# Performance work log

Measured on AMD Instinct MI355X. Metric: run time of the kernel, lower is better.

## Reference

```python
import jax, jax.numpy as jnp
import numpy as np

N_NODES = 50000
N_EDGES = 200000
NODE_F = 64
EDGE_F = 16
HID = 32
LAT = 16


def _glorot(key, shape):
    fan_in, fan_out = shape[0], shape[1]
    lim = np.sqrt(6.0 / (fan_in + fan_out))
    return jax.random.uniform(key, shape, jnp.float32, -lim, lim)


def setup_inputs() -> dict:
    key = jax.random.key(0)
    ks = jax.random.split(key, 24)
    inp = {
        "x": jax.random.normal(ks[0], (N_NODES, NODE_F), jnp.float32),
        "edge_index": jax.random.randint(ks[1], (2, N_EDGES), 0, N_NODES, jnp.int64),
        "edge_attr": jax.random.normal(ks[2], (N_EDGES, EDGE_F), jnp.float32),
        # encoder input projection
        "lin_in_w": _glorot(ks[3], (NODE_F, HID)),
        "lin_in_b": jnp.zeros((HID,), jnp.float32),
        # 3 edge MLPs (stacked over layer axis)
        "edge_w1": jnp.stack([_glorot(ks[4 + i], (EDGE_F, HID)) for i in range(3)]),
        "edge_b1": jnp.zeros((3, HID), jnp.float32),
        "edge_w2": jnp.stack([_glorot(ks[7 + i], (HID, HID * HID)) * 0.1 for i in range(3)]),
        "edge_b2": jnp.zeros((3, HID * HID), jnp.float32),
        # 3 NNConv root weights + biases
        "root_w": jnp.stack([_glorot(ks[10 + i], (HID, HID)) for i in range(3)]),
        "root_b": jnp.zeros((3, HID), jnp.float32),
        # encoder output projection
        "lin_out_w": _glorot(ks[13], (HID, LAT)),
        "lin_out_b": jnp.zeros((LAT,), jnp.float32),
        # node decoder MLP
        "dec_w1": _glorot(ks[14], (LAT, HID)),
        "dec_b1": jnp.zeros((HID,), jnp.float32),
        "dec_w2": _glorot(ks[15], (HID, NODE_F)),
        "dec_b2": jnp.zeros((NODE_F,), jnp.float32),
    }
    return inp


def _nnconv(x, src, dst, edge_attr, w1, b1, w2, b2, root_w, root_b):
    # per-edge weight matrix from edge MLP: [E, H, H]
    h = jax.nn.relu(edge_attr @ w1 + b1)
    w_e = (h @ w2 + b2).reshape(-1, HID, HID)
    # gather source features, per-edge matmul: [E, H]
    msg = jnp.einsum("eh,eho->eo", x[src], w_e)
    # scatter-mean to destinations
    agg = jax.ops.segment_sum(msg, dst, num_segments=N_NODES)
    cnt = jax.ops.segment_sum(jnp.ones((msg.shape[0], 1), x.dtype), dst, num_segments=N_NODES)
    agg = agg / jnp.maximum(cnt, 1.0)
    # root weight + bias
    return agg + x @ root_w + root_b


def reference(x, edge_index, edge_attr, lin_in_w, lin_in_b, edge_w1, edge_b1,
              edge_w2, edge_b2, root_w, root_b, lin_out_w, lin_out_b,
              dec_w1, dec_b1, dec_w2, dec_b2):
    src, dst = edge_index[0], edge_index[1]
    h = jax.nn.relu(x @ lin_in_w + lin_in_b)
    for i in range(3):  # fixed number of conv layers (dropout is identity in eval)
        h = _nnconv(h, src, dst, edge_attr, edge_w1[i], edge_b1[i],
                    edge_w2[i], edge_b2[i], root_w[i], root_b[i])
        h = jax.nn.relu(h)
    z = h @ lin_out_w + lin_out_b
    # node decoder
    d = jax.nn.relu(z @ dec_w1 + dec_b1)
    return d @ dec_w2 + dec_b2
```

## Files before the change

kernel.cpp:

```cpp
#include <hip/hip_runtime.h>
#include <hip/hip_bf16.h>
#include <stdint.h>

#define N_NODES 50000
#define N_EDGES 200000
#define NODE_F 64
#define EDGE_F 16
#define HID 32
#define LAT 16
#define W2A_L 33792
#define SCAN_BLOCKS 196

typedef __attribute__((ext_vector_type(8))) short short8;
typedef __attribute__((ext_vector_type(4))) float f32x4;
typedef __attribute__((ext_vector_type(2))) float f32x2;

static __device__ __forceinline__ unsigned short bfbits(float f) {
  union { __hip_bfloat16 h; unsigned short s; } c; c.h = __float2bfloat16(f); return c.s;
}
static __device__ __forceinline__ unsigned pkt(f32x2 v) {
  return __builtin_amdgcn_perm(__float_as_uint(v.y), __float_as_uint(v.x), 0x07060302u);
}
union AFrag { short8 v; unsigned u[4]; };

__global__ void k_prep(const float* __restrict__ ew2, const float* __restrict__ eb2,
                       const float* __restrict__ ew1,
                       unsigned short* __restrict__ w2a,
                       unsigned short* __restrict__ w1p,
                       int* __restrict__ deg,
                       float* __restrict__ agg) {
  int g = blockIdx.x*256 + threadIdx.x;
  int l = g / W2A_L;
  int r = g % W2A_L;
  int k = r >> 10;
  int r2 = r & 1023;
  int mt = r2 >> 9;
  int ln = (r2 >> 3) & 63;
  int j  = r2 & 7;
  int h  = (ln >> 4)*8 + j;
  int m  = mt*16 + (ln & 15);
  float v = (k < 32) ? ew2[(size_t)l*32768 + k*1024 + h*32 + m]
                     : eb2[(size_t)l*1024 + h*32 + m];
  w2a[g] = bfbits(v);
  if (g < N_NODES) deg[g] = 0;
  {
    float4 z4 = make_float4(0.f,0.f,0.f,0.f);
    float4* a4 = (float4*)agg;
    for (int i = g; i < N_NODES*HID/4; i += 101376) a4[i] = z4;
  }
  if (g < 3*2*64*8) {
    int l2 = g >> 10;
    int r3 = g & 1023;
    int nt = r3 >> 9;
    int ln2 = (r3 >> 3) & 63;
    int j2  = r3 & 7;
    int kgr = ln2 >> 4;
    float w = (kgr < 2) ? ew1[(size_t)l2*512 + (kgr*8 + j2)*32 + nt*16 + (ln2 & 15)] : 0.f;
    w1p[g] = bfbits(w);
  }
}

__global__ void k_hist(const int* __restrict__ ei, int* __restrict__ deg) {
  int t = blockIdx.x*256 + threadIdx.x;
  if (t >= N_EDGES) return;
  int d = ei[N_EDGES + t];
  d = min(max(d, 0), N_NODES-1);
  atomicAdd(&deg[d], 1);
}

__global__ __launch_bounds__(256) void k_scan1(const int* __restrict__ deg,
                                               int* __restrict__ off,
                                               int* __restrict__ bsum) {
  __shared__ int s[256];
  const int tid = threadIdx.x;
  const int t = blockIdx.x*256 + tid;
  int d = (t < N_NODES) ? deg[t] : 0;
  s[tid] = d; __syncthreads();
  int v = d;
  #pragma unroll
  for (int ofs = 1; ofs < 256; ofs <<= 1) {
    int w = (tid >= ofs) ? s[tid-ofs] : 0;
    __syncthreads();
    v += w; s[tid] = v;
    __syncthreads();
  }
  if (t < N_NODES) off[t] = v - d;
  if (tid == 255) bsum[blockIdx.x] = v;
}

__global__ __launch_bounds__(256) void k_scan23(int* __restrict__ off,
                                                const int* __restrict__ bsum,
                                                int* __restrict__ cursor) {
  __shared__ int sPref;
  const int tid = threadIdx.x;
  const int b = blockIdx.x;
  if (tid < 64) {
    int acc = 0;
    for (int i = tid; i < b; i += 64) acc += bsum[i];
    #pragma unroll
    for (int o = 32; o; o >>= 1) acc += __shfl_down(acc, o);
    if (tid == 0) sPref = acc;
  }
  __syncthreads();
  int pref = sPref;
  int t = b*256 + tid;
  if (t < N_NODES) {
    off[t] += pref;
    cursor[t] = 0;
  }
  if (t == 0) off[N_NODES] = N_EDGES;
}

__global__ void k_scatter(const int* __restrict__ ei, const int* __restrict__ off,
                          int* __restrict__ cursor,
                          int* __restrict__ csr_src, int* __restrict__ csr_eid,
                          int* __restrict__ csr_dst) {
  int t = blockIdx.x*256 + threadIdx.x;
  if (t >= N_EDGES) return;
  int d = ei[N_EDGES + t];
  d = min(max(d, 0), N_NODES-1);
  int s = ei[t];
  s = min(max(s, 0), N_NODES-1);
  int pos = off[d] + atomicAdd(&cursor[d], 1);
  csr_src[pos] = s;
  csr_eid[pos] = t;
  csr_dst[pos] = d;
}

__global__ void k_lin_in(const float* __restrict__ x,
                         const float* __restrict__ W,
                         const float* __restrict__ b,
                         float* __restrict__ h) {
  __shared__ float Ws[NODE_F*HID];
  __shared__ float bs[HID];
  for (int i = threadIdx.x; i < NODE_F*HID; i += 256) Ws[i] = W[i];
  if (threadIdx.x < HID) bs[threadIdx.x] = b[threadIdx.x];
  __syncthreads();
  int t = blockIdx.x*256 + threadIdx.x;
  if (t >= N_NODES*HID) return;
  int n = t >> 5, o = t & 31;
  const float4* xp = (const float4*)(x + (size_t)n*NODE_F);
  float acc = bs[o];
  #pragma unroll
  for (int j = 0; j < NODE_F/4; j++) {
    float4 v = xp[j];
    acc = fmaf(v.x, Ws[(4*j+0)*HID+o], acc);
    acc = fmaf(v.y, Ws[(4*j+1)*HID+o], acc);
    acc = fmaf(v.z, Ws[(4*j+2)*HID+o], acc);
    acc = fmaf(v.w, Ws[(4*j+3)*HID+o], acc);
  }
  h[t] = fmaxf(acc, 0.f);
}

__global__ __launch_bounds__(256) void k_msgagg(const float* __restrict__ hin,
                                                const float* __restrict__ ea,
                                                const unsigned short* __restrict__ w1pl,
                                                const float* __restrict__ b1,
                                                const unsigned short* __restrict__ w2al,
                                                const int* __restrict__ csr_src,
                                                const int* __restrict__ csr_eid,
                                                const int* __restrict__ csr_dst,
                                                const int* __restrict__ off,
                                                float* __restrict__ agg) {
  __shared__ float sHE[256*33];
  __shared__ int   sSRC[256];
  __shared__ int   sEID[256];
  const int tid = threadIdx.x;
  const int be  = blockIdx.x*256;
  const int wv   = tid >> 6;
  const int lane = tid & 63;
  const int nn   = lane & 15;
  const int quad = lane >> 4;
  const int wbase = wv*64;

  {
    int el = wbase + lane;
    int pos = min(be + el, N_EDGES-1);
    sSRC[el] = csr_src[pos];
    sEID[el] = csr_eid[pos];
    sHE[el*33 + 32] = 1.0f;
  }

  {
    short8 wb0 = *(const short8*)(w1pl + lane*8);
    short8 wb1 = *(const short8*)(w1pl + 512 + lane*8);
    f32x4 z = {0.f,0.f,0.f,0.f};
    float bv0 = b1[nn], bv1 = b1[nn + 16];
    #pragma unroll
    for (int t = 0; t < 4; t++) {
      AFrag a;
      if (quad < 2) {
        int e = sEID[wbase + t*16 + nn];
        const float4* p = (const float4*)(ea + (size_t)e*EDGE_F + quad*8);
        float4 u = p[0], v = p[1];
        a.u[0] = pkt(f32x2{u.x,u.y}); a.u[1] = pkt(f32x2{u.z,u.w});
        a.u[2] = pkt(f32x2{v.x,v.y}); a.u[3] = pkt(f32x2{v.z,v.w});
      } else {
        #pragma unroll
        for (int i = 0; i < 4; i++) a.u[i] = 0u;
      }
      f32x4 h0 = __builtin_amdgcn_mfma_f32_16x16x32_bf16(a.v, wb0, z, 0, 0, 0);
      f32x4 h1 = __builtin_amdgcn_mfma_f32_16x16x32_bf16(a.v, wb1, z, 0, 0, 0);
      #pragma unroll
      for (int r = 0; r < 4; r++) {
        int ro = (wbase + t*16 + quad*4 + r)*33;
        sHE[ro + nn]      = fmaxf(h0[r] + bv0, 0.f);
        sHE[ro + 16 + nn] = fmaxf(h1[r] + bv1, 0.f);
      }
    }
  }

  short8 bx[4];
  #pragma unroll
  for (int t = 0; t < 4; t++) {
    int si = sSRC[wbase + t*16 + nn];
    const float4* p = (const float4*)(hin + (size_t)si*HID + quad*8);
    float4 a = p[0], b = p[1];
    AFrag f;
    f.u[0] = pkt(f32x2{a.x,a.y}); f.u[1] = pkt(f32x2{a.z,a.w});
    f.u[2] = pkt(f32x2{b.x,b.y}); f.u[3] = pkt(f32x2{b.z,b.w});
    bx[t] = f.v;
  }

  f32x4 c0[4], c1[4];
  #pragma unroll
  for (int t = 0; t < 4; t++) { c0[t] = f32x4{0.f,0.f,0.f,0.f}; c1[t] = c0[t]; }
  const f32x4 zz = {0.f,0.f,0.f,0.f};

  const unsigned short* ap = w2al + (unsigned)lane*8;
  const float* heR[4];
  #pragma unroll
  for (int t = 0; t < 4; t++) heR[t] = sHE + (wbase + t*16 + nn)*33;

  short8 sa0[3], sa1[3];
  float  sh[3][4];
  #pragma unroll
  for (int j = 0; j < 3; j++) {
    sa0[j] = *(const short8*)(ap + j*1024);
    sa1[j] = *(const short8*)(ap + j*1024 + 512);
    #pragma unroll
    for (int t = 0; t < 4; t++) sh[j][t] = heR[t][j];
  }

  #pragma unroll 1
  for (int base = 0; base < 30; base += 3) {
    #pragma unroll
    for (int j = 0; j < 3; j++) {
      const int kk = base + j;
      short8 a0 = sa0[j], a1 = sa1[j];
      #pragma unroll
      for (int t = 0; t < 4; t++) {
        f32x4 u0 = __builtin_amdgcn_mfma_f32_16x16x32_bf16(a0, bx[t], zz, 0, 0, 0);
        f32x4 u1 = __builtin_amdgcn_mfma_f32_16x16x32_bf16(a1, bx[t], zz, 0, 0, 0);
        float hk = sh[j][t];
        #pragma unroll
        for (int r = 0; r < 4; r++) {
          c0[t][r] = fmaf(hk, u0[r], c0[t][r]);
          c1[t][r] = fmaf(hk, u1[r], c1[t][r]);
        }
      }
      sa0[j] = *(const short8*)(ap + (kk+3)*1024);
      sa1[j] = *(const short8*)(ap + (kk+3)*1024 + 512);
      #pragma unroll
      for (int t = 0; t < 4; t++) sh[j][t] = heR[t][kk+3];
    }
  }
  #pragma unroll
  for (int j = 0; j < 3; j++) {
    short8 a0 = sa0[j], a1 = sa1[j];
    #pragma unroll
    for (int t = 0; t < 4; t++) {
      f32x4 u0 = __builtin_amdgcn_mfma_f32_16x16x32_bf16(a0, bx[t], zz, 0, 0, 0);
      f32x4 u1 = __builtin_amdgcn_mfma_f32_16x16x32_bf16(a1, bx[t], zz, 0, 0, 0);
      float hk = sh[j][t];
      #pragma unroll
      for (int r = 0; r < 4; r++) {
        c0[t][r] = fmaf(hk, u0[r], c0[t][r]);
        c1[t][r] = fmaf(hk, u1[r], c1[t][r]);
      }
    }
  }

  #pragma unroll
  for (int t = 0; t < 4; t++) {
    int ro = (wbase + t*16 + nn)*33 + quad*4;
    sHE[ro + 0]  = c0[t][0]; sHE[ro + 1]  = c0[t][1];
    sHE[ro + 2]  = c0[t][2]; sHE[ro + 3]  = c0[t][3];
    sHE[ro + 16] = c1[t][0]; sHE[ro + 17] = c1[t][1];
    sHE[ro + 18] = c1[t][2]; sHE[ro + 19] = c1[t][3];
  }
  __syncthreads();

  const int s    = be;
  const int wend = s + 256;
  const int nF = csr_dst[min(s,       N_EDGES-1)];
  const int nL = csr_dst[min(s + 255, N_EDGES-1)];
  for (int basei = 0; basei <= nL - nF; basei += 32) {
    int idx = basei + (tid >> 3);
    int n = nF + idx;
    if (n <= nL) {
      int oc = tid & 7;
      int s0 = off[n], s1 = off[n+1];
      int lo = max(s0, s) - s;
      int hi = min(s1, wend) - s;
      float a0 = 0.f, a1 = 0.f, a2 = 0.f, a3 = 0.f;
      for (int j = lo; j < hi; j++) {
        const float* row = sHE + j*33 + oc*4;
        a0 += row[0]; a1 += row[1]; a2 += row[2]; a3 += row[3];
      }
      float* dst = agg + (size_t)n*HID + oc*4;
      if (s0 >= s && s1 <= wend) {
        *(float4*)dst = make_float4(a0, a1, a2, a3);
      } else {
        atomicAdd(dst + 0, a0); atomicAdd(dst + 1, a1);
        atomicAdd(dst + 2, a2); atomicAdd(dst + 3, a3);
      }
    }
  }
}

__global__ void k_root(float* __restrict__ agg,
                       const int* __restrict__ off,
                       const float* __restrict__ hin,
                       const float* __restrict__ rw,
                       const float* __restrict__ rb,
                       float* __restrict__ hout) {
  __shared__ float rws[HID*HID];
  __shared__ float rbs[HID];
  for (int i = threadIdx.x; i < HID*HID; i += 256) rws[i] = rw[i];
  if (threadIdx.x < HID) rbs[threadIdx.x] = rb[threadIdx.x];
  __syncthreads();
  int t = blockIdx.x*256 + threadIdx.x;
  if (t >= N_NODES*8) return;
  int n = t >> 3, oc = t & 7;
  float4* ap = (float4*)(agg + (size_t)n*HID);
  float4 av = ap[oc];
  float inv = 1.f / fmaxf((float)(off[n+1] - off[n]), 1.f);
  float a0 = fmaf(av.x, inv, rbs[oc*4+0]);
  float a1 = fmaf(av.y, inv, rbs[oc*4+1]);
  float a2 = fmaf(av.z, inv, rbs[oc*4+2]);
  float a3 = fmaf(av.w, inv, rbs[oc*4+3]);
  const float4* hp = (const float4*)(hin + (size_t)n*HID);
  #pragma unroll
  for (int jq = 0; jq < 8; jq++) {
    float4 hv = hp[jq];
    #pragma unroll
    for (int c = 0; c < 4; c++) {
      int j = jq*4 + c;
      float h = (c==0)?hv.x:(c==1)?hv.y:(c==2)?hv.z:hv.w;
      const float4* rp = (const float4*)(rws + j*HID + oc*4);
      float4 r = rp[0];
      a0 = fmaf(h, r.x, a0);
      a1 = fmaf(h, r.y, a1);
      a2 = fmaf(h, r.z, a2);
      a3 = fmaf(h, r.w, a3);
    }
  }
  ((float4*)(hout + (size_t)n*HID))[oc] =
      make_float4(fmaxf(a0,0.f), fmaxf(a1,0.f), fmaxf(a2,0.f), fmaxf(a3,0.f));
  ap[oc] = make_float4(0.f, 0.f, 0.f, 0.f);
}

__global__ void k_decoder(const float* __restrict__ agg,
                          const int* __restrict__ off,
                          const float* __restrict__ h,
                          const float* __restrict__ rw, const float* __restrict__ rb,
                          const float* __restrict__ lo_w, const float* __restrict__ lo_b,
                          const float* __restrict__ d1_w, const float* __restrict__ d1_b,
                          const float* __restrict__ d2_w, const float* __restrict__ d2_b,
                          float* __restrict__ out) {
  __shared__ float rws[HID*HID], rbs[HID];
  __shared__ float lows[HID*LAT], lobs[LAT], d1s[LAT*HID], d1bs[HID], d2s[HID*NODE_F], d2bs[NODE_F];
  for (int i = threadIdx.x; i < HID*HID; i += 256) rws[i] = rw[i];
  for (int i = threadIdx.x; i < HID; i += 256) rbs[i] = rb[i];
  for (int i = threadIdx.x; i < HID*LAT; i += 256) lows[i] = lo_w[i];
  for (int i = threadIdx.x; i < LAT; i += 256) lobs[i] = lo_b[i];
  for (int i = threadIdx.x; i < LAT*HID; i += 256) d1s[i] = d1_w[i];
  for (int i = threadIdx.x; i < HID; i += 256) d1bs[i] = d1_b[i];
  for (int i = threadIdx.x; i < HID*NODE_F; i += 256) d2s[i] = d2_w[i];
  for (int i = threadIdx.x; i < NODE_F; i += 256) d2bs[i] = d2_b[i];
  __syncthreads();
  int n = blockIdx.x*256 + threadIdx.x;
  if (n >= N_NODES) return;
  float hv[HID], av[HID];
  const float4* hp = (const float4*)(h + (size_t)n*HID);
  const float4* ap = (const float4*)(agg + (size_t)n*HID);
  #pragma unroll
  for (int i = 0; i < HID/4; i++) {
    float4 v = hp[i]; hv[4*i]=v.x; hv[4*i+1]=v.y; hv[4*i+2]=v.z; hv[4*i+3]=v.w;
    float4 a = ap[i]; av[4*i]=a.x; av[4*i+1]=a.y; av[4*i+2]=a.z; av[4*i+3]=a.w;
  }
  float inv = 1.f / fmaxf((float)(off[n+1] - off[n]), 1.f);
  float hr[HID];
  #pragma unroll 4
  for (int o = 0; o < HID; o++) {
    float a = fmaf(av[o], inv, rbs[o]);
    #pragma unroll
    for (int j = 0; j < HID; j++) a = fmaf(hv[j], rws[j*HID+o], a);
    hr[o] = fmaxf(a, 0.f);
  }
  float z[LAT];
  #pragma unroll
  for (int o = 0; o < LAT; o++) {
    float a = lobs[o];
    #pragma unroll
    for (int j = 0; j < HID; j++) a = fmaf(hr[j], lows[j*LAT+o], a);
    z[o] = a;
  }
  float d[HID];
  #pragma unroll
  for (int o = 0; o < HID; o++) {
    float a = d1bs[o];
    #pragma unroll
    for (int j = 0; j < LAT; j++) a = fmaf(z[j], d1s[j*HID+o], a);
    d[o] = fmaxf(a, 0.f);
  }
  float* op = out + (size_t)n*NODE_F;
  #pragma unroll 8
  for (int o = 0; o < NODE_F; o++) {
    float a = d2bs[o];
    #pragma unroll
    for (int j = 0; j < HID; j++) a = fmaf(d[j], d2s[j*NODE_F+o], a);
    op[o] = a;
  }
}

extern "C" void kernel_launch(void* const* d_in, const int* in_sizes, int n_in,
                              void* d_out, int out_size, void* d_ws, size_t ws_size,
                              hipStream_t stream) {
  const float* x   = (const float*)d_in[0];
  const int*   ei  = (const int*)d_in[1];
  const float* ea  = (const float*)d_in[2];
  const float* liw = (const float*)d_in[3];
  const float* lib = (const float*)d_in[4];
  const float* ew1 = (const float*)d_in[5];
  const float* eb1 = (const float*)d_in[6];
  const float* ew2 = (const float*)d_in[7];
  const float* eb2 = (const float*)d_in[8];
  const float* rw  = (const float*)d_in[9];
  const float* rb  = (const float*)d_in[10];
  const float* low = (const float*)d_in[11];
  const float* lob = (const float*)d_in[12];
  const float* d1w = (const float*)d_in[13];
  const float* d1b = (const float*)d_in[14];
  const float* d2w = (const float*)d_in[15];
  const float* d2b = (const float*)d_in[16];
  float* out = (float*)d_out;

  float* h0   = (float*)d_ws;
  float* h1   = h0  + (size_t)N_NODES*HID;
  float* agg  = h1  + (size_t)N_NODES*HID;
  int*  deg   = (int*)(agg + (size_t)N_NODES*HID);
  int*  off   = deg + N_NODES;
  int*  cursor= off + N_NODES + 16;
  int*  csrs  = cursor + N_NODES;
  int*  csre  = csrs + N_EDGES;
  int*  csrd  = csre + N_EDGES;
  int*  bsum  = csrd + N_EDGES;
  unsigned short* w2a = (unsigned short*)(bsum + 256);
  unsigned short* w1p = w2a + 3*W2A_L;

  k_prep<<<(3*W2A_L)/256, 256, 0, stream>>>(ew2, eb2, ew1, w2a, w1p, deg, agg);
  k_hist<<<(N_EDGES + 255)/256, 256, 0, stream>>>(ei, deg);
  k_scan1<<<SCAN_BLOCKS, 256, 0, stream>>>(deg, off, bsum);
  k_scan23<<<SCAN_BLOCKS, 256, 0, stream>>>(off, bsum, cursor);
  k_scatter<<<(N_EDGES + 255)/256, 256, 0, stream>>>(ei, off, cursor, csrs, csre, csrd);

  k_lin_in<<<(N_NODES*HID + 255)/256, 256, 0, stream>>>(x, liw, lib, h0);

  k_msgagg<<<(N_EDGES + 255)/256, 256, 0, stream>>>(h0, ea, w1p, eb1,
      w2a, csrs, csre, csrd, off, agg);
  k_root<<<(N_NODES*8 + 255)/256, 256, 0, stream>>>(agg, off, h0, rw, rb, h1);
  k_msgagg<<<(N_EDGES + 255)/256, 256, 0, stream>>>(h1, ea, w1p + 1024, eb1 + HID,
      w2a + (size_t)W2A_L, csrs, csre, csrd, off, agg);
  k_root<<<(N_NODES*8 + 255)/256, 256, 0, stream>>>(agg, off, h1, rw + HID*HID, rb + HID, h0);
  k_msgagg<<<(N_EDGES + 255)/256, 256, 0, stream>>>(h0, ea, w1p + 2048, eb1 + 2*HID,
      w2a + (size_t)2*W2A_L, csrs, csre, csrd, off, agg);
  k_decoder<<<(N_NODES + 255)/256, 256, 0, stream>>>(agg, off, h0,
      rw + 2*HID*HID, rb + 2*HID, low, lob, d1w, d1b, d2w, d2b, out);
}
```

Baseline: 284.7 us.

## Fuse whole GNN pipeline into one persistent cooperative kernel with grid syncs

Replaces the chain of separate launches (prep, histogram, scan, scatter, input projection, three message/aggregate layers, root updates and decoder) with one cooperative kernel of 512 blocks. Stages are separated by grid-wide barriers, and the work loops are grid-strided. The goal is to remove per-launch overhead and the idle gaps between small kernels. The trade-off is the cost of about ten grid barriers, a fixed grid that processes the 782 message tiles in uneven rounds, and occupancy limited by the launch bound. The old multi-kernel path stays as a fallback if the cooperative launch fails.

```diff
diff --git a/kernel.cpp b/kernel.cpp
--- a/kernel.cpp
+++ b/kernel.cpp
@@ -1,4 +1,5 @@
 #include <hip/hip_runtime.h>
+#include <hip/hip_cooperative_groups.h>
 #include <hip/hip_bf16.h>
 #include <stdint.h>
 
@@ -10,6 +11,11 @@
 #define LAT 16
 #define W2A_L 33792
 #define SCAN_BLOCKS 196
+#define NTILES 782
+#define FUSED_BLOCKS 512
+#define FUSED_THREADS (FUSED_BLOCKS*256)
+
+namespace cg = cooperative_groups;
 
 typedef __attribute__((ext_vector_type(8))) short short8;
 typedef __attribute__((ext_vector_type(4))) float f32x4;
@@ -23,31 +29,25 @@
 }
 union AFrag { short8 v; unsigned u[4]; };
 
-__global__ void k_prep(const float* __restrict__ ew2, const float* __restrict__ eb2,
-                       const float* __restrict__ ew1,
-                       unsigned short* __restrict__ w2a,
-                       unsigned short* __restrict__ w1p,
-                       int* __restrict__ deg,
-                       float* __restrict__ agg) {
-  int g = blockIdx.x*256 + threadIdx.x;
-  int l = g / W2A_L;
-  int r = g % W2A_L;
-  int k = r >> 10;
-  int r2 = r & 1023;
-  int mt = r2 >> 9;
-  int ln = (r2 >> 3) & 63;
-  int j  = r2 & 7;
-  int h  = (ln >> 4)*8 + j;
-  int m  = mt*16 + (ln & 15);
-  float v = (k < 32) ? ew2[(size_t)l*32768 + k*1024 + h*32 + m]
-                     : eb2[(size_t)l*1024 + h*32 + m];
-  w2a[g] = bfbits(v);
+
+__device__ __forceinline__ void dev_prep_item(int g,
+    const float* ew2, const float* eb2, const float* ew1,
+    unsigned short* w2a, unsigned short* w1p, int* deg) {
+  if (g < 3*W2A_L) {
+    int l = g / W2A_L;
+    int r = g % W2A_L;
+    int k = r >> 10;
+    int r2 = r & 1023;
+    int mt = r2 >> 9;
+    int ln = (r2 >> 3) & 63;
+    int j  = r2 & 7;
+    int h  = (ln >> 4)*8 + j;
+    int m  = mt*16 + (ln & 15);
+    float v = (k < 32) ? ew2[(size_t)l*32768 + k*1024 + h*32 + m]
+                       : eb2[(size_t)l*1024 + h*32 + m];
+    w2a[g] = bfbits(v);
+  }
   if (g < N_NODES) deg[g] = 0;
-  {
-    float4 z4 = make_float4(0.f,0.f,0.f,0.f);
-    float4* a4 = (float4*)agg;
-    for (int i = g; i < N_NODES*HID/4; i += 101376) a4[i] = z4;
-  }
   if (g < 3*2*64*8) {
     int l2 = g >> 10;
     int r3 = g & 1023;
@@ -60,84 +60,8 @@
   }
 }
 
-__global__ void k_hist(const int* __restrict__ ei, int* __restrict__ deg) {
-  int t = blockIdx.x*256 + threadIdx.x;
-  if (t >= N_EDGES) return;
-  int d = ei[N_EDGES + t];
-  d = min(max(d, 0), N_NODES-1);
-  atomicAdd(&deg[d], 1);
-}
-
-__global__ __launch_bounds__(256) void k_scan1(const int* __restrict__ deg,
-                                               int* __restrict__ off,
-                                               int* __restrict__ bsum) {
-  __shared__ int s[256];
-  const int tid = threadIdx.x;
-  const int t = blockIdx.x*256 + tid;
-  int d = (t < N_NODES) ? deg[t] : 0;
-  s[tid] = d; __syncthreads();
-  int v = d;
-  #pragma unroll
-  for (int ofs = 1; ofs < 256; ofs <<= 1) {
-    int w = (tid >= ofs) ? s[tid-ofs] : 0;
-    __syncthreads();
-    v += w; s[tid] = v;
-    __syncthreads();
-  }
-  if (t < N_NODES) off[t] = v - d;
-  if (tid == 255) bsum[blockIdx.x] = v;
-}
-
-__global__ __launch_bounds__(256) void k_scan23(int* __restrict__ off,
-                                                const int* __restrict__ bsum,
-                                                int* __restrict__ cursor) {
-  __shared__ int sPref;
-  const int tid = threadIdx.x;
-  const int b = blockIdx.x;
-  if (tid < 64) {
-    int acc = 0;
-    for (int i = tid; i < b; i += 64) acc += bsum[i];
-    #pragma unroll
-    for (int o = 32; o; o >>= 1) acc += __shfl_down(acc, o);
-    if (tid == 0) sPref = acc;
-  }
-  __syncthreads();
-  int pref = sPref;
-  int t = b*256 + tid;
-  if (t < N_NODES) {
-    off[t] += pref;
-    cursor[t] = 0;
-  }
-  if (t == 0) off[N_NODES] = N_EDGES;
-}
-
-__global__ void k_scatter(const int* __restrict__ ei, const int* __restrict__ off,
-                          int* __restrict__ cursor,
-                          int* __restrict__ csr_src, int* __restrict__ csr_eid,
-                          int* __restrict__ csr_dst) {
-  int t = blockIdx.x*256 + threadIdx.x;
-  if (t >= N_EDGES) return;
-  int d = ei[N_EDGES + t];
-  d = min(max(d, 0), N_NODES-1);
-  int s = ei[t];
-  s = min(max(s, 0), N_NODES-1);
-  int pos = off[d] + atomicAdd(&cursor[d], 1);
-  csr_src[pos] = s;
-  csr_eid[pos] = t;
-  csr_dst[pos] = d;
-}
-
-__global__ void k_lin_in(const float* __restrict__ x,
-                         const float* __restrict__ W,
-                         const float* __restrict__ b,
-                         float* __restrict__ h) {
-  __shared__ float Ws[NODE_F*HID];
-  __shared__ float bs[HID];
-  for (int i = threadIdx.x; i < NODE_F*HID; i += 256) Ws[i] = W[i];
-  if (threadIdx.x < HID) bs[threadIdx.x] = b[threadIdx.x];
-  __syncthreads();
-  int t = blockIdx.x*256 + threadIdx.x;
-  if (t >= N_NODES*HID) return;
+__device__ __forceinline__ void dev_lin_item(int t, const float* x,
+    const float* Ws, const float* bs, float* h) {
   int n = t >> 5, o = t & 31;
   const float4* xp = (const float4*)(x + (size_t)n*NODE_F);
   float acc = bs[o];
@@ -152,21 +76,68 @@
   h[t] = fmaxf(acc, 0.f);
 }
 
-__global__ __launch_bounds__(256) void k_msgagg(const float* __restrict__ hin,
-                                                const float* __restrict__ ea,
-                                                const unsigned short* __restrict__ w1pl,
-                                                const float* __restrict__ b1,
-                                                const unsigned short* __restrict__ w2al,
-                                                const int* __restrict__ csr_src,
-                                                const int* __restrict__ csr_eid,
-                                                const int* __restrict__ csr_dst,
-                                                const int* __restrict__ off,
-                                                float* __restrict__ agg) {
-  __shared__ float sHE[256*33];
-  __shared__ int   sSRC[256];
-  __shared__ int   sEID[256];
-  const int tid = threadIdx.x;
-  const int be  = blockIdx.x*256;
+__device__ __forceinline__ void dev_hist_item(int t, const int* ei, int* deg) {
+  int d = ei[N_EDGES + t];
+  d = min(max(d, 0), N_NODES-1);
+  atomicAdd(&deg[d], 1);
+}
+
+__device__ __forceinline__ void dev_scan1(int b, int tid, int* s,
+    const int* deg, int* off, int* bsum) {
+  int t = b*256 + tid;
+  int d = (t < N_NODES) ? deg[t] : 0;
+  s[tid] = d; __syncthreads();
+  int v = d;
+  #pragma unroll
+  for (int ofs = 1; ofs < 256; ofs <<= 1) {
+    int w = (tid >= ofs) ? s[tid-ofs] : 0;
+    __syncthreads();
+    v += w; s[tid] = v;
+    __syncthreads();
+  }
+  if (t < N_NODES) off[t] = v - d;
+  if (tid == 255) bsum[b] = v;
+}
+
+__device__ __forceinline__ void dev_scan23(int b, int tid, int* sPref,
+    int* off, const int* bsum, int* cursor) {
+  if (tid < 64) {
+    int acc = 0;
+    for (int i = tid; i < b; i += 64) acc += bsum[i];
+    #pragma unroll
+    for (int o = 32; o; o >>= 1) acc += __shfl_down(acc, o);
+    if (tid == 0) sPref[0] = acc;
+  }
+  __syncthreads();
+  int pref = sPref[0];
+  int t = b*256 + tid;
+  if (t < N_NODES) {
+    off[t] += pref;
+    cursor[t] = 0;
+  }
+  if (t == 0) off[N_NODES] = N_EDGES;
+}
+
+__device__ __forceinline__ void dev_scatter_item(int t, const int* ei,
+    const int* off, int* cursor, int* csrs, int* csre, int* csrd) {
+  int d = ei[N_EDGES + t];
+  d = min(max(d, 0), N_NODES-1);
+  int s = ei[t];
+  s = min(max(s, 0), N_NODES-1);
+  int pos = off[d] + atomicAdd(&cursor[d], 1);
+  csrs[pos] = s;
+  csre[pos] = t;
+  csrd[pos] = d;
+}
+
+__device__ __forceinline__ void dev_msgagg_tile(
+    float* sHE, int* sSRC, int* sEID, int tile, int tid,
+    const float* hin, const float* ea,
+    const unsigned short* w1pl, const float* b1,
+    const unsigned short* w2al,
+    const int* csr_src, const int* csr_eid, const int* csr_dst,
+    const int* off, float* agg) {
+  const int be  = tile*256;
   const int wv   = tid >> 6;
   const int lane = tid & 63;
   const int nn   = lane & 15;
@@ -319,6 +290,261 @@
   }
 }
 
+__device__ __forceinline__ void dev_root_item(int t, float* agg, const int* off,
+    const float* hin, const float* rws, const float* rbs, float* hout) {
+  int n = t >> 3, oc = t & 7;
+  float4* ap = (float4*)(agg + (size_t)n*HID);
+  float4 av = ap[oc];
+  float inv = 1.f / fmaxf((float)(off[n+1] - off[n]), 1.f);
+  float a0 = fmaf(av.x, inv, rbs[oc*4+0]);
+  float a1 = fmaf(av.y, inv, rbs[oc*4+1]);
+  float a2 = fmaf(av.z, inv, rbs[oc*4+2]);
+  float a3 = fmaf(av.w, inv, rbs[oc*4+3]);
+  const float4* hp = (const float4*)(hin + (size_t)n*HID);
+  #pragma unroll
+  for (int jq = 0; jq < 8; jq++) {
+    float4 hv = hp[jq];
+    #pragma unroll
+    for (int c = 0; c < 4; c++) {
+      int j = jq*4 + c;
+      float h = (c==0)?hv.x:(c==1)?hv.y:(c==2)?hv.z:hv.w;
+      const float4* rp = (const float4*)(rws + j*HID + oc*4);
+      float4 r = rp[0];
+      a0 = fmaf(h, r.x, a0);
+      a1 = fmaf(h, r.y, a1);
+      a2 = fmaf(h, r.z, a2);
+      a3 = fmaf(h, r.w, a3);
+    }
+  }
+  ((float4*)(hout + (size_t)n*HID))[oc] =
+      make_float4(fmaxf(a0,0.f), fmaxf(a1,0.f), fmaxf(a2,0.f), fmaxf(a3,0.f));
+  ap[oc] = make_float4(0.f, 0.f, 0.f, 0.f);
+}
+
+__device__ __forceinline__ void dev_decoder_node(int n,
+    const float* agg, const int* off, const float* h,
+    const float* rws, const float* rbs,
+    const float* lows, const float* lobs,
+    const float* d1s, const float* d1bs,
+    const float* d2s, const float* d2bs,
+    float* out) {
+  float hv[HID], av[HID];
+  const float4* hp = (const float4*)(h + (size_t)n*HID);
+  const float4* ap = (const float4*)(agg + (size_t)n*HID);
+  #pragma unroll
+  for (int i = 0; i < HID/4; i++) {
+    float4 v = hp[i]; hv[4*i]=v.x; hv[4*i+1]=v.y; hv[4*i+2]=v.z; hv[4*i+3]=v.w;
+    float4 a = ap[i]; av[4*i]=a.x; av[4*i+1]=a.y; av[4*i+2]=a.z; av[4*i+3]=a.w;
+  }
+  float inv = 1.f / fmaxf((float)(off[n+1] - off[n]), 1.f);
+  float hr[HID];
+  #pragma unroll 4
+  for (int o = 0; o < HID; o++) {
+    float a = fmaf(av[o], inv, rbs[o]);
+    #pragma unroll
+    for (int j = 0; j < HID; j++) a = fmaf(hv[j], rws[j*HID+o], a);
+    hr[o] = fmaxf(a, 0.f);
+  }
+  float z[LAT];
+  #pragma unroll
+  for (int o = 0; o < LAT; o++) {
+    float a = lobs[o];
+    #pragma unroll
+    for (int j = 0; j < HID; j++) a = fmaf(hr[j], lows[j*LAT+o], a);
+    z[o] = a;
+  }
+  float d[HID];
+  #pragma unroll
+  for (int o = 0; o < HID; o++) {
+    float a = d1bs[o];
+    #pragma unroll
+    for (int j = 0; j < LAT; j++) a = fmaf(z[j], d1s[j*HID+o], a);
+    d[o] = fmaxf(a, 0.f);
+  }
+  float* op = out + (size_t)n*NODE_F;
+  #pragma unroll 8
+  for (int o = 0; o < NODE_F; o++) {
+    float a = d2bs[o];
+    #pragma unroll
+    for (int j = 0; j < HID; j++) a = fmaf(d[j], d2s[j*NODE_F+o], a);
+    op[o] = a;
+  }
+}
+
+
+struct FusedArgs {
+  const float *x, *ea;
+  const int *ei;
+  const float *liw, *lib, *eb1, *rw, *rb, *low, *lob, *d1w, *d1b, *d2w, *d2b;
+  const float *ew1, *ew2, *eb2;
+  float *out, *h0, *h1, *agg;
+  int *deg, *off, *cursor, *csrs, *csre, *csrd, *bsum;
+  unsigned short *w2a, *w1p;
+};
+
+__global__ __launch_bounds__(256, 2) void k_fused(FusedArgs a) {
+  __shared__ float smem[256*33 + 512];
+  cg::grid_group grid = cg::this_grid();
+  const int tid = threadIdx.x;
+  const int bid = blockIdx.x;
+  const int gidx = bid*256 + tid;
+
+  {
+    float* Ws = smem;
+    float* bs = smem + NODE_F*HID;
+    for (int i = tid; i < NODE_F*HID; i += 256) Ws[i] = a.liw[i];
+    if (tid < HID) bs[tid] = a.lib[tid];
+    __syncthreads();
+    dev_prep_item(gidx, a.ew2, a.eb2, a.ew1, a.w2a, a.w1p, a.deg);
+    float4 z4 = make_float4(0.f,0.f,0.f,0.f);
+    float4* a4 = (float4*)a.agg;
+    for (int i = gidx; i < N_NODES*HID/4; i += FUSED_THREADS) a4[i] = z4;
+    for (int t = gidx; t < N_NODES*HID; t += FUSED_THREADS)
+      dev_lin_item(t, a.x, Ws, bs, a.h0);
+  }
+  grid.sync();
+
+  for (int t = gidx; t < N_EDGES; t += FUSED_THREADS) dev_hist_item(t, a.ei, a.deg);
+  grid.sync();
+
+  if (bid < SCAN_BLOCKS) dev_scan1(bid, tid, (int*)smem, a.deg, a.off, a.bsum);
+  grid.sync();
+
+  if (bid < SCAN_BLOCKS) dev_scan23(bid, tid, (int*)smem, a.off, a.bsum, a.cursor);
+  grid.sync();
+
+  for (int t = gidx; t < N_EDGES; t += FUSED_THREADS)
+    dev_scatter_item(t, a.ei, a.off, a.cursor, a.csrs, a.csre, a.csrd);
+  grid.sync();
+
+  float* sHE = smem;
+  int* sSRC = (int*)(smem + 256*33);
+  int* sEID = sSRC + 256;
+  const float* hin = a.h0;
+  float* hout = a.h1;
+  #pragma unroll 1
+  for (int l = 0; l < 3; l++) {
+    const unsigned short* w1pl = a.w1p + (size_t)l*1024;
+    const float* b1 = a.eb1 + l*HID;
+    const unsigned short* w2al = a.w2a + (size_t)l*W2A_L;
+    #pragma unroll 1
+    for (int t5 = bid; t5 < NTILES; t5 += gridDim.x) {
+      __syncthreads();
+      dev_msgagg_tile(sHE, sSRC, sEID, t5, tid, hin, a.ea, w1pl, b1, w2al,
+                      a.csrs, a.csre, a.csrd, a.off, a.agg);
+    }
+    grid.sync();
+    if (l < 2) {
+      float* rws = smem;
+      float* rbs = smem + HID*HID;
+      for (int i = tid; i < HID*HID; i += 256) rws[i] = a.rw[(size_t)l*HID*HID + i];
+      if (tid < HID) rbs[tid] = a.rb[l*HID + tid];
+      __syncthreads();
+      for (int t = gidx; t < N_NODES*8; t += FUSED_THREADS)
+        dev_root_item(t, a.agg, a.off, hin, rws, rbs, hout);
+      grid.sync();
+      const float* tmp = hin; hin = hout; hout = (float*)tmp;
+    }
+  }
+
+  {
+    float* rws  = smem;
+    float* rbs  = smem + 1024;
+    float* lows = smem + 1056;
+    float* lobs = smem + 1568;
+    float* d1s  = smem + 1584;
+    float* d1bs = smem + 2096;
+    float* d2s  = smem + 2128;
+    float* d2bs = smem + 4176;
+    for (int i = tid; i < HID*HID; i += 256) rws[i] = a.rw[(size_t)2*HID*HID + i];
+    for (int i = tid; i < HID; i += 256) rbs[i] = a.rb[2*HID + i];
+    for (int i = tid; i < HID*LAT; i += 256) lows[i] = a.low[i];
+    for (int i = tid; i < LAT; i += 256) lobs[i] = a.lob[i];
+    for (int i = tid; i < LAT*HID; i += 256) d1s[i] = a.d1w[i];
+    for (int i = tid; i < HID; i += 256) d1bs[i] = a.d1b[i];
+    for (int i = tid; i < HID*NODE_F; i += 256) d2s[i] = a.d2w[i];
+    for (int i = tid; i < NODE_F; i += 256) d2bs[i] = a.d2b[i];
+    __syncthreads();
+    if (gidx < N_NODES)
+      dev_decoder_node(gidx, a.agg, a.off, hin, rws, rbs, lows, lobs,
+                       d1s, d1bs, d2s, d2bs, a.out);
+  }
+}
+
+
+__global__ void k_prep(const float* __restrict__ ew2, const float* __restrict__ eb2,
+                       const float* __restrict__ ew1,
+                       unsigned short* __restrict__ w2a,
+                       unsigned short* __restrict__ w1p,
+                       int* __restrict__ deg,
+                       float* __restrict__ agg) {
+  int g = blockIdx.x*256 + threadIdx.x;
+  dev_prep_item(g, ew2, eb2, ew1, w2a, w1p, deg);
+  float4 z4 = make_float4(0.f,0.f,0.f,0.f);
+  float4* a4 = (float4*)agg;
+  for (int i = g; i < N_NODES*HID/4; i += 101376) a4[i] = z4;
+}
+
+__global__ void k_hist(const int* __restrict__ ei, int* __restrict__ deg) {
+  int t = blockIdx.x*256 + threadIdx.x;
+  if (t >= N_EDGES) return;
+  dev_hist_item(t, ei, deg);
+}
+
+__global__ __launch_bounds__(256) void k_scan1(const int* __restrict__ deg,
+                                               int* __restrict__ off,
+                                               int* __restrict__ bsum) {
+  __shared__ int s[256];
+  dev_scan1(blockIdx.x, threadIdx.x, s, deg, off, bsum);
+}
+
+__global__ __launch_bounds__(256) void k_scan23(int* __restrict__ off,
+                                                const int* __restrict__ bsum,
+                                                int* __restrict__ cursor) {
+  __shared__ int sPref[1];
+  dev_scan23(blockIdx.x, threadIdx.x, sPref, off, bsum, cursor);
+}
+
+__global__ void k_scatter(const int* __restrict__ ei, const int* __restrict__ off,
+                          int* __restrict__ cursor,
+                          int* __restrict__ csr_src, int* __restrict__ csr_eid,
+                          int* __restrict__ csr_dst) {
+  int t = blockIdx.x*256 + threadIdx.x;
+  if (t >= N_EDGES) return;
+  dev_scatter_item(t, ei, off, cursor, csr_src, csr_eid, csr_dst);
+}
+
+__global__ void k_lin_in(const float* __restrict__ x,
+                         const float* __restrict__ W,
+                         const float* __restrict__ b,
+                         float* __restrict__ h) {
+  __shared__ float Ws[NODE_F*HID];
+  __shared__ float bs[HID];
+  for (int i = threadIdx.x; i < NODE_F*HID; i += 256) Ws[i] = W[i];
+  if (threadIdx.x < HID) bs[threadIdx.x] = b[threadIdx.x];
+  __syncthreads();
+  int t = blockIdx.x*256 + threadIdx.x;
+  if (t >= N_NODES*HID) return;
+  dev_lin_item(t, x, Ws, bs, h);
+}
+
+__global__ __launch_bounds__(256) void k_msgagg(const float* __restrict__ hin,
+                                                const float* __restrict__ ea,
+                                                const unsigned short* __restrict__ w1pl,
+                                                const float* __restrict__ b1,
+                                                const unsigned short* __restrict__ w2al,
+                                                const int* __restrict__ csr_src,
+                                                const int* __restrict__ csr_eid,
+                                                const int* __restrict__ csr_dst,
+                                                const int* __restrict__ off,
+                                                float* __restrict__ agg) {
+  __shared__ float sHE[256*33];
+  __shared__ int   sSRC[256];
+  __shared__ int   sEID[256];
+  dev_msgagg_tile(sHE, sSRC, sEID, blockIdx.x, threadIdx.x, hin, ea, w1pl, b1,
+                  w2al, csr_src, csr_eid, csr_dst, off, agg);
+}
+
 __global__ void k_root(float* __restrict__ agg,
                        const int* __restrict__ off,
                        const float* __restrict__ hin,
@@ -332,33 +558,7 @@
   __syncthreads();
   int t = blockIdx.x*256 + threadIdx.x;
   if (t >= N_NODES*8) return;
-  int n = t >> 3, oc = t & 7;
-  float4* ap = (float4*)(agg + (size_t)n*HID);
-  float4 av = ap[oc];
-  float inv = 1.f / fmaxf((float)(off[n+1] - off[n]), 1.f);
-  float a0 = fmaf(av.x, inv, rbs[oc*4+0]);
-  float a1 = fmaf(av.y, inv, rbs[oc*4+1]);
-  float a2 = fmaf(av.z, inv, rbs[oc*4+2]);
-  float a3 = fmaf(av.w, inv, rbs[oc*4+3]);
-  const float4* hp = (const float4*)(hin + (size_t)n*HID);
-  #pragma unroll
-  for (int jq = 0; jq < 8; jq++) {
-    float4 hv = hp[jq];
-    #pragma unroll
-    for (int c = 0; c < 4; c++) {
-      int j = jq*4 + c;
-      float h = (c==0)?hv.x:(c==1)?hv.y:(c==2)?hv.z:hv.w;
-      const float4* rp = (const float4*)(rws + j*HID + oc*4);
-      float4 r = rp[0];
-      a0 = fmaf(h, r.x, a0);
-      a1 = fmaf(h, r.y, a1);
-      a2 = fmaf(h, r.z, a2);
-      a3 = fmaf(h, r.w, a3);
-    }
-  }
-  ((float4*)(hout + (size_t)n*HID))[oc] =
-      make_float4(fmaxf(a0,0.f), fmaxf(a1,0.f), fmaxf(a2,0.f), fmaxf(a3,0.f));
-  ap[oc] = make_float4(0.f, 0.f, 0.f, 0.f);
+  dev_root_item(t, agg, off, hin, rws, rbs, hout);
 }
 
 __global__ void k_decoder(const float* __restrict__ agg,
@@ -382,47 +582,7 @@
   __syncthreads();
   int n = blockIdx.x*256 + threadIdx.x;
   if (n >= N_NODES) return;
-  float hv[HID], av[HID];
-  const float4* hp = (const float4*)(h + (size_t)n*HID);
-  const float4* ap = (const float4*)(agg + (size_t)n*HID);
-  #pragma unroll
-  for (int i = 0; i < HID/4; i++) {
-    float4 v = hp[i]; hv[4*i]=v.x; hv[4*i+1]=v.y; hv[4*i+2]=v.z; hv[4*i+3]=v.w;
-    float4 a = ap[i]; av[4*i]=a.x; av[4*i+1]=a.y; av[4*i+2]=a.z; av[4*i+3]=a.w;
-  }
-  float inv = 1.f / fmaxf((float)(off[n+1] - off[n]), 1.f);
-  float hr[HID];
-  #pragma unroll 4
-  for (int o = 0; o < HID; o++) {
-    float a = fmaf(av[o], inv, rbs[o]);
-    #pragma unroll
-    for (int j = 0; j < HID; j++) a = fmaf(hv[j], rws[j*HID+o], a);
-    hr[o] = fmaxf(a, 0.f);
-  }
-  float z[LAT];
-  #pragma unroll
-  for (int o = 0; o < LAT; o++) {
-    float a = lobs[o];
-    #pragma unroll
-    for (int j = 0; j < HID; j++) a = fmaf(hr[j], lows[j*LAT+o], a);
-    z[o] = a;
-  }
-  float d[HID];
-  #pragma unroll
-  for (int o = 0; o < HID; o++) {
-    float a = d1bs[o];
-    #pragma unroll
-    for (int j = 0; j < LAT; j++) a = fmaf(z[j], d1s[j*HID+o], a);
-    d[o] = fmaxf(a, 0.f);
-  }
-  float* op = out + (size_t)n*NODE_F;
-  #pragma unroll 8
-  for (int o = 0; o < NODE_F; o++) {
-    float a = d2bs[o];
-    #pragma unroll
-    for (int j = 0; j < HID; j++) a = fmaf(d[j], d2s[j*NODE_F+o], a);
-    op[o] = a;
-  }
+  dev_decoder_node(n, agg, off, h, rws, rbs, lows, lobs, d1s, d1bs, d2s, d2bs, out);
 }
 
 extern "C" void kernel_launch(void* const* d_in, const int* in_sizes, int n_in,
@@ -460,6 +620,22 @@
   unsigned short* w2a = (unsigned short*)(bsum + 256);
   unsigned short* w1p = w2a + 3*W2A_L;
 
+  FusedArgs fa;
+  fa.x = x; fa.ea = ea; fa.ei = ei;
+  fa.liw = liw; fa.lib = lib; fa.eb1 = eb1; fa.rw = rw; fa.rb = rb;
+  fa.low = low; fa.lob = lob; fa.d1w = d1w; fa.d1b = d1b; fa.d2w = d2w; fa.d2b = d2b;
+  fa.ew1 = ew1; fa.ew2 = ew2; fa.eb2 = eb2;
+  fa.out = out; fa.h0 = h0; fa.h1 = h1; fa.agg = agg;
+  fa.deg = deg; fa.off = off; fa.cursor = cursor;
+  fa.csrs = csrs; fa.csre = csre; fa.csrd = csrd; fa.bsum = bsum;
+  fa.w2a = w2a; fa.w1p = w1p;
+
+  void* kp[] = { (void*)&fa };
+  hipError_t err = hipLaunchCooperativeKernel((const void*)k_fused,
+      dim3(FUSED_BLOCKS), dim3(256), kp, 0, stream);
+  if (err == hipSuccess) return;
+  (void)hipGetLastError();
+
   k_prep<<<(3*W2A_L)/256, 256, 0, stream>>>(ew2, eb2, ew1, w2a, w1p, deg, agg);
   k_hist<<<(N_EDGES + 255)/256, 256, 0, stream>>>(ei, deg);
   k_scan1<<<SCAN_BLOCKS, 256, 0, stream>>>(deg, off, bsum);
@@ -468,13 +644,13 @@
 
   k_lin_in<<<(N_NODES*HID + 255)/256, 256, 0, stream>>>(x, liw, lib, h0);
 
-  k_msgagg<<<(N_EDGES + 255)/256, 256, 0, stream>>>(h0, ea, w1p, eb1,
+  k_msgagg<<<NTILES, 256, 0, stream>>>(h0, ea, w1p, eb1,
       w2a, csrs, csre, csrd, off, agg);
   k_root<<<(N_NODES*8 + 255)/256, 256, 0, stream>>>(agg, off, h0, rw, rb, h1);
-  k_msgagg<<<(N_EDGES + 255)/256, 256, 0, stream>>>(h1, ea, w1p + 1024, eb1 + HID,
+  k_msgagg<<<NTILES, 256, 0, stream>>>(h1, ea, w1p + 1024, eb1 + HID,
       w2a + (size_t)W2A_L, csrs, csre, csrd, off, agg);
   k_root<<<(N_NODES*8 + 255)/256, 256, 0, stream>>>(agg, off, h1, rw + HID*HID, rb + HID, h0);
-  k_msgagg<<<(N_EDGES + 255)/256, 256, 0, stream>>>(h0, ea, w1p + 2048, eb1 + 2*HID,
+  k_msgagg<<<NTILES, 256, 0, stream>>>(h0, ea, w1p + 2048, eb1 + 2*HID,
       w2a + (size_t)2*W2A_L, csrs, csre, csrd, off, agg);
   k_decoder<<<(N_NODES + 255)/256, 256, 0, stream>>>(agg, off, h0,
       rw + 2*HID*HID, rb + 2*HID, low, lob, d1w, d1b, d2w, d2b, out);
```

Measured after the change: 857.7 us. +201.3%, slower.

## Fuse preprocessing kernels into one launch and use single-block scan

Applied to the files above, without the earlier changes.

Merges weight repacking, degree histogram, agg zeroing and the input projection into one grid-stride kernel. The deg zeroing moves to a memset because the histogram now runs in the same kernel. The two-pass block scan becomes a single 1024-thread block, with each thread scanning 49 elements serially. This cuts several launches and one scan pass, but the single-block scan serialises 50k elements on one CU and the fused kernel has fewer threads for the lin_in work.

```diff
diff --git a/kernel.cpp b/kernel.cpp
--- a/kernel.cpp
+++ b/kernel.cpp
@@ -9,7 +9,10 @@
 #define HID 32
 #define LAT 16
 #define W2A_L 33792
-#define SCAN_BLOCKS 196
+#define NTILES 782
+#define MEGA_BLOCKS 1024
+#define MEGA_THREADS (MEGA_BLOCKS*256)
+#define CHUNK 49
 
 typedef __attribute__((ext_vector_type(8))) short short8;
 typedef __attribute__((ext_vector_type(4))) float f32x4;
@@ -23,30 +26,34 @@
 }
 union AFrag { short8 v; unsigned u[4]; };
 
-__global__ void k_prep(const float* __restrict__ ew2, const float* __restrict__ eb2,
-                       const float* __restrict__ ew1,
-                       unsigned short* __restrict__ w2a,
-                       unsigned short* __restrict__ w1p,
-                       int* __restrict__ deg,
-                       float* __restrict__ agg) {
-  int g = blockIdx.x*256 + threadIdx.x;
-  int l = g / W2A_L;
-  int r = g % W2A_L;
-  int k = r >> 10;
-  int r2 = r & 1023;
-  int mt = r2 >> 9;
-  int ln = (r2 >> 3) & 63;
-  int j  = r2 & 7;
-  int h  = (ln >> 4)*8 + j;
-  int m  = mt*16 + (ln & 15);
-  float v = (k < 32) ? ew2[(size_t)l*32768 + k*1024 + h*32 + m]
-                     : eb2[(size_t)l*1024 + h*32 + m];
-  w2a[g] = bfbits(v);
-  if (g < N_NODES) deg[g] = 0;
-  {
-    float4 z4 = make_float4(0.f,0.f,0.f,0.f);
-    float4* a4 = (float4*)agg;
-    for (int i = g; i < N_NODES*HID/4; i += 101376) a4[i] = z4;
+__global__ __launch_bounds__(256) void k_mega(
+    const float* __restrict__ ew2, const float* __restrict__ eb2,
+    const float* __restrict__ ew1,
+    const int* __restrict__ ei,
+    const float* __restrict__ x, const float* __restrict__ liw,
+    const float* __restrict__ lib,
+    unsigned short* __restrict__ w2a, unsigned short* __restrict__ w1p,
+    int* __restrict__ deg, float* __restrict__ agg, float* __restrict__ h0) {
+  __shared__ float Ws[NODE_F*HID];
+  __shared__ float bs[HID];
+  for (int i = threadIdx.x; i < NODE_F*HID; i += 256) Ws[i] = liw[i];
+  if (threadIdx.x < HID) bs[threadIdx.x] = lib[threadIdx.x];
+  __syncthreads();
+  const int g = blockIdx.x*256 + threadIdx.x;
+
+  if (g < 3*W2A_L) {
+    int l = g / W2A_L;
+    int r = g % W2A_L;
+    int k = r >> 10;
+    int r2 = r & 1023;
+    int mt = r2 >> 9;
+    int ln = (r2 >> 3) & 63;
+    int j  = r2 & 7;
+    int h  = (ln >> 4)*8 + j;
+    int m  = mt*16 + (ln & 15);
+    float v = (k < 32) ? ew2[(size_t)l*32768 + k*1024 + h*32 + m]
+                       : eb2[(size_t)l*1024 + h*32 + m];
+    w2a[g] = bfbits(v);
   }
   if (g < 3*2*64*8) {
     int l2 = g >> 10;
@@ -58,57 +65,63 @@
     float w = (kgr < 2) ? ew1[(size_t)l2*512 + (kgr*8 + j2)*32 + nt*16 + (ln2 & 15)] : 0.f;
     w1p[g] = bfbits(w);
   }
-}
-
-__global__ void k_hist(const int* __restrict__ ei, int* __restrict__ deg) {
-  int t = blockIdx.x*256 + threadIdx.x;
-  if (t >= N_EDGES) return;
-  int d = ei[N_EDGES + t];
-  d = min(max(d, 0), N_NODES-1);
-  atomicAdd(&deg[d], 1);
-}
-
-__global__ __launch_bounds__(256) void k_scan1(const int* __restrict__ deg,
-                                               int* __restrict__ off,
-                                               int* __restrict__ bsum) {
-  __shared__ int s[256];
+  if (g < N_EDGES) {
+    int d = ei[N_EDGES + g];
+    d = min(max(d, 0), N_NODES-1);
+    atomicAdd(&deg[d], 1);
+  }
+  {
+    float4 z4 = make_float4(0.f,0.f,0.f,0.f);
+    float4* a4 = (float4*)agg;
+    for (int i = g; i < N_NODES*HID/4; i += MEGA_THREADS) a4[i] = z4;
+  }
+  for (int t = g; t < N_NODES*HID; t += MEGA_THREADS) {
+    int n = t >> 5, o = t & 31;
+    const float4* xp = (const float4*)(x + (size_t)n*NODE_F);
+    float acc = bs[o];
+    #pragma unroll
+    for (int j = 0; j < NODE_F/4; j++) {
+      float4 v = xp[j];
+      acc = fmaf(v.x, Ws[(4*j+0)*HID+o], acc);
+      acc = fmaf(v.y, Ws[(4*j+1)*HID+o], acc);
+      acc = fmaf(v.z, Ws[(4*j+2)*HID+o], acc);
+      acc = fmaf(v.w, Ws[(4*j+3)*HID+o], acc);
+    }
+    h0[t] = fmaxf(acc, 0.f);
+  }
+}
+
+__global__ __launch_bounds__(1024) void k_scan_one(const int* __restrict__ deg,
+                                                   int* __restrict__ off,
+                                                   int* __restrict__ cursor) {
+  __shared__ int s[1024];
   const int tid = threadIdx.x;
-  const int t = blockIdx.x*256 + tid;
-  int d = (t < N_NODES) ? deg[t] : 0;
-  s[tid] = d; __syncthreads();
-  int v = d;
-  #pragma unroll
-  for (int ofs = 1; ofs < 256; ofs <<= 1) {
+  const int lo = tid*CHUNK;
+  int loc[CHUNK];
+  int sum = 0;
+  #pragma unroll
+  for (int c = 0; c < CHUNK; c++) {
+    int i = lo + c;
+    int d = (i < N_NODES) ? deg[i] : 0;
+    loc[c] = sum;
+    sum += d;
+  }
+  s[tid] = sum; __syncthreads();
+  int v = sum;
+  #pragma unroll
+  for (int ofs = 1; ofs < 1024; ofs <<= 1) {
     int w = (tid >= ofs) ? s[tid-ofs] : 0;
     __syncthreads();
     v += w; s[tid] = v;
     __syncthreads();
   }
-  if (t < N_NODES) off[t] = v - d;
-  if (tid == 255) bsum[blockIdx.x] = v;
-}
-
-__global__ __launch_bounds__(256) void k_scan23(int* __restrict__ off,
-                                                const int* __restrict__ bsum,
-                                                int* __restrict__ cursor) {
-  __shared__ int sPref;
-  const int tid = threadIdx.x;
-  const int b = blockIdx.x;
-  if (tid < 64) {
-    int acc = 0;
-    for (int i = tid; i < b; i += 64) acc += bsum[i];
-    #pragma unroll
-    for (int o = 32; o; o >>= 1) acc += __shfl_down(acc, o);
-    if (tid == 0) sPref = acc;
-  }
-  __syncthreads();
-  int pref = sPref;
-  int t = b*256 + tid;
-  if (t < N_NODES) {
-    off[t] += pref;
-    cursor[t] = 0;
-  }
-  if (t == 0) off[N_NODES] = N_EDGES;
+  const int base = v - sum;
+  #pragma unroll
+  for (int c = 0; c < CHUNK; c++) {
+    int i = lo + c;
+    if (i < N_NODES) { off[i] = base + loc[c]; cursor[i] = 0; }
+  }
+  if (tid == 1023) off[N_NODES] = N_EDGES;
 }
 
 __global__ void k_scatter(const int* __restrict__ ei, const int* __restrict__ off,
@@ -125,31 +138,6 @@
   csr_src[pos] = s;
   csr_eid[pos] = t;
   csr_dst[pos] = d;
-}
-
-__global__ void k_lin_in(const float* __restrict__ x,
-                         const float* __restrict__ W,
-                         const float* __restrict__ b,
-                         float* __restrict__ h) {
-  __shared__ float Ws[NODE_F*HID];
-  __shared__ float bs[HID];
-  for (int i = threadIdx.x; i < NODE_F*HID; i += 256) Ws[i] = W[i];
-  if (threadIdx.x < HID) bs[threadIdx.x] = b[threadIdx.x];
-  __syncthreads();
-  int t = blockIdx.x*256 + threadIdx.x;
-  if (t >= N_NODES*HID) return;
-  int n = t >> 5, o = t & 31;
-  const float4* xp = (const float4*)(x + (size_t)n*NODE_F);
-  float acc = bs[o];
-  #pragma unroll
-  for (int j = 0; j < NODE_F/4; j++) {
-    float4 v = xp[j];
-    acc = fmaf(v.x, Ws[(4*j+0)*HID+o], acc);
-    acc = fmaf(v.y, Ws[(4*j+1)*HID+o], acc);
-    acc = fmaf(v.z, Ws[(4*j+2)*HID+o], acc);
-    acc = fmaf(v.w, Ws[(4*j+3)*HID+o], acc);
-  }
-  h[t] = fmaxf(acc, 0.f);
 }
 
 __global__ __launch_bounds__(256) void k_msgagg(const float* __restrict__ hin,
@@ -456,25 +444,22 @@
   int*  csrs  = cursor + N_NODES;
   int*  csre  = csrs + N_EDGES;
   int*  csrd  = csre + N_EDGES;
-  int*  bsum  = csrd + N_EDGES;
-  unsigned short* w2a = (unsigned short*)(bsum + 256);
+  unsigned short* w2a = (unsigned short*)(csrd + N_EDGES);
   unsigned short* w1p = w2a + 3*W2A_L;
 
-  k_prep<<<(3*W2A_L)/256, 256, 0, stream>>>(ew2, eb2, ew1, w2a, w1p, deg, agg);
-  k_hist<<<(N_EDGES + 255)/256, 256, 0, stream>>>(ei, deg);
-  k_scan1<<<SCAN_BLOCKS, 256, 0, stream>>>(deg, off, bsum);
-  k_scan23<<<SCAN_BLOCKS, 256, 0, stream>>>(off, bsum, cursor);
-  k_scatter<<<(N_EDGES + 255)/256, 256, 0, stream>>>(ei, off, cursor, csrs, csre, csrd);
-
-  k_lin_in<<<(N_NODES*HID + 255)/256, 256, 0, stream>>>(x, liw, lib, h0);
-
-  k_msgagg<<<(N_EDGES + 255)/256, 256, 0, stream>>>(h0, ea, w1p, eb1,
+  hipMemsetAsync(deg, 0, (size_t)N_NODES*sizeof(int), stream);
+  k_mega<<<MEGA_BLOCKS, 256, 0, stream>>>(ew2, eb2, ew1, ei, x, liw, lib,
+                                          w2a, w1p, deg, agg, h0);
+  k_scan_one<<<1, 1024, 0, stream>>>(deg, off, cursor);
+  k_scatter<<<NTILES, 256, 0, stream>>>(ei, off, cursor, csrs, csre, csrd);
+
+  k_msgagg<<<NTILES, 256, 0, stream>>>(h0, ea, w1p, eb1,
       w2a, csrs, csre, csrd, off, agg);
   k_root<<<(N_NODES*8 + 255)/256, 256, 0, stream>>>(agg, off, h0, rw, rb, h1);
-  k_msgagg<<<(N_EDGES + 255)/256, 256, 0, stream>>>(h1, ea, w1p + 1024, eb1 + HID,
+  k_msgagg<<<NTILES, 256, 0, stream>>>(h1, ea, w1p + 1024, eb1 + HID,
       w2a + (size_t)W2A_L, csrs, csre, csrd, off, agg);
   k_root<<<(N_NODES*8 + 255)/256, 256, 0, stream>>>(agg, off, h1, rw + HID*HID, rb + HID, h0);
-  k_msgagg<<<(N_EDGES + 255)/256, 256, 0, stream>>>(h0, ea, w1p + 2048, eb1 + 2*HID,
+  k_msgagg<<<NTILES, 256, 0, stream>>>(h0, ea, w1p + 2048, eb1 + 2*HID,
       w2a + (size_t)2*W2A_L, csrs, csre, csrd, off, agg);
   k_decoder<<<(N_NODES + 255)/256, 256, 0, stream>>>(agg, off, h0,
       rw + 2*HID*HID, rb + 2*HID, low, lob, d1w, d1b, d2w, d2b, out);
```

Result: slower. 353.2 us (+24.1%).
